# Performance work log

Hardware: AMD Instinct MI355X
Metric: run time of the kernel (lower is better)

Reference implementation:

```python
import jax, jax.numpy as jnp
import numpy as np

D_IN, H1, H2, H3 = 1024, 512, 256, 128  # embedding MLP dims
D_CBP = 2048                             # compact bilinear pooling output dim
H_C = 1024                               # comparator hidden dim
CLASSES = 10
B = 16384
SLOPE = 0.2  # LeakyReLU negative slope


def _lrelu(x):
    return jnp.where(x >= 0, x, SLOPE * x)


def _embed(x, W1, b1, W2, b2, W3, b3):
    x = _lrelu(x @ W1 + b1)
    x = _lrelu(x @ W2 + b2)
    x = _lrelu(x @ W3 + b3)
    return x  # [B, 128]


def setup_inputs() -> dict:
    key = jax.random.key(0)
    ks = jax.random.split(key, 16)

    def lin(k, fan_in, fan_out):
        bound = 1.0 / np.sqrt(fan_in)
        kw, kb = jax.random.split(k)
        W = jax.random.uniform(kw, (fan_in, fan_out), jnp.float32, -bound, bound)
        b = jax.random.uniform(kb, (fan_out,), jnp.float32, -bound, bound)
        return W, b

    W1, b1 = lin(ks[0], D_IN, H1)
    W2, b2 = lin(ks[1], H1, H2)
    W3, b3 = lin(ks[2], H2, H3)
    Wc1, bc1 = lin(ks[3], D_CBP, H_C)
    Wc2, bc2 = lin(ks[4], H_C, CLASSES)

    X = jax.random.normal(ks[5], (B, D_IN), jnp.float32)
    Centers = jax.random.normal(ks[6], (B, D_IN), jnp.float32)

    # count-sketch hashes (int constants) and +-1 signs (float buffers)
    h1 = jax.random.randint(ks[7], (H3,), 0, D_CBP, jnp.int32)
    h2 = jax.random.randint(ks[8], (H3,), 0, D_CBP, jnp.int32)
    s1 = jnp.sign(jax.random.normal(ks[9], (H3,), jnp.float32)) + (jax.random.normal(ks[9], (H3,)) == 0)
    s2 = jnp.sign(jax.random.normal(ks[10], (H3,), jnp.float32)) + (jax.random.normal(ks[10], (H3,)) == 0)

    return {"X": X, "Centers": Centers,
            "W1": W1, "b1": b1, "W2": W2, "b2": b2, "W3": W3, "b3": b3,
            "h1": h1, "s1": s1, "h2": h2, "s2": s2,
            "Wc1": Wc1, "bc1": bc1, "Wc2": Wc2, "bc2": bc2}


def _cbp(x, y, h1, s1, h2, s2):
    # count-sketch via tiny dense sketch matrices [128, 2048]
    M1 = jnp.zeros((H3, D_CBP), x.dtype).at[jnp.arange(H3), h1].set(s1)
    M2 = jnp.zeros((H3, D_CBP), y.dtype).at[jnp.arange(H3), h2].set(s2)
    sk1 = x @ M1  # [B, 2048]
    sk2 = y @ M2
    # circular convolution via real FFT
    return jnp.fft.irfft(jnp.fft.rfft(sk1, axis=-1) * jnp.fft.rfft(sk2, axis=-1), n=D_CBP, axis=-1)


def reference(X, Centers, W1, b1, W2, b2, W3, b3, h1, s1, h2, s2, Wc1, bc1, Wc2, bc2):
    ex = _embed(X, W1, b1, W2, b2, W3, b3)        # [B, 128]
    ec = _embed(Centers, W1, b1, W2, b2, W3, b3)  # [B, 128]
    cbp = _cbp(ex, ec, h1, s1, h2, s2)            # [B, 2048]
    z = _lrelu(cbp @ Wc1 + bc1)                   # [B, 1024]
    logits = z @ Wc2 + bc2                        # [B, classes]
    return jax.nn.softmax(logits, axis=1)
```

## Files before the change

kernel.cpp:

```cpp
#include <hip/hip_runtime.h>
#include <hip/hip_bf16.h>
#include <math.h>

#define BATCH   16384
#define D_IN    1024
#define H1_DIM  512
#define H2_DIM  256
#define H3_DIM  128
#define D_CBP   2048
#define H_C     1024
#define CLASSES 10
#define SLOPE   0.2f

#define NK_PAD  1088
#define NF      (2 * NK_PAD)
#define NF_USED 2080

typedef short v8s __attribute__((ext_vector_type(8)));
typedef float v4f __attribute__((ext_vector_type(4)));
typedef unsigned short u16;
typedef unsigned int   u32;

__device__ __forceinline__ float b2f(unsigned short u) {
  return __uint_as_float(((unsigned)u) << 16);
}
__device__ __forceinline__ u16 f2b(float f) {
  __hip_bfloat16 h = __float2bfloat16(f);
  return __builtin_bit_cast(unsigned short, h);
}

__device__ __forceinline__ float2 twiddle(int idx) {
  const float ang = 6.2831853071795864769f * (float)idx / 2048.f;
  return make_float2(__cosf(ang), __sinf(ang));
}

__device__ __forceinline__ void g2l16(const void* g, void* l) {
  __builtin_amdgcn_global_load_lds(
      (const __attribute__((address_space(1))) void*)g,
      (__attribute__((address_space(3))) void*)l, 16, 0, 0);
}

__global__ __launch_bounds__(256) void gemm_bf16(
    const u16* __restrict__ A,
    const u16* __restrict__ Bt,
    const float* __restrict__ bias,
    u16* __restrict__ C,
    int M, int N, int K, int lda, int ldb, float slope)
{
  __shared__ __align__(16) short Asb[5][128 * 32];
  __shared__ __align__(16) short Bsb[5][128 * 32];

  const int tid  = threadIdx.x;
  const int wave = tid >> 6, lane = tid & 63;
  const int wm = wave >> 1, wn = wave & 1;
  const int u = lane & 15, quad = lane >> 4;

  const int nwg = gridDim.x * gridDim.y;
  int id = blockIdx.y * gridDim.x + blockIdx.x;
  if ((nwg & 7) == 0) id = (id & 7) * (nwg >> 3) + (id >> 3);
  const int m0 = (id / gridDim.x) * 128, n0 = (id % gridDim.x) * 128;

  const int g_log = ((lane & 3) - ((lane >> 3) & 3)) & 3;
  const int srow  = wave * 32 + (lane >> 2);
  const u16* gA0 = A  + (size_t)(m0 + srow)      * lda + g_log * 8;
  const u16* gA1 = A  + (size_t)(m0 + srow + 16) * lda + g_log * 8;
  const u16* gB0 = Bt + (size_t)(n0 + srow)      * ldb + g_log * 8;
  const u16* gB1 = Bt + (size_t)(n0 + srow + 16) * ldb + g_log * 8;
  const int lo0 = (wave * 32)      * 32;
  const int lo1 = (wave * 32 + 16) * 32;

  const int gran = (quad + (u >> 1)) & 3;
  int offA[4], offB[4];
#pragma unroll
  for (int i = 0; i < 4; ++i) {
    offA[i] = (wm * 64 + i * 16 + u) * 32 + gran * 8;
    offB[i] = (wn * 64 + i * 16 + u) * 32 + gran * 8;
  }

  v4f acc[4][4];
#pragma unroll
  for (int i = 0; i < 4; ++i)
#pragma unroll
    for (int j = 0; j < 4; ++j) acc[i][j] = (v4f){0.f, 0.f, 0.f, 0.f};

  const int nsteps = K >> 5;

  auto stage = [&](int s, int buf) {
    const int k0 = s * 32;
    g2l16(gA0 + k0, &Asb[buf][lo0]);
    g2l16(gA1 + k0, &Asb[buf][lo1]);
    g2l16(gB0 + k0, &Bsb[buf][lo0]);
    g2l16(gB1 + k0, &Bsb[buf][lo1]);
  };

  stage(0, 0);
  if (nsteps > 1) stage(1, 1);
  if (nsteps > 2) stage(2, 2);

  int cb = 0, sb = 3;
  for (int t = 0; t < nsteps; ++t) {
    if (t + 3 < nsteps) stage(t + 3, sb);

    const int rem = nsteps - 1 - t;
    if (rem >= 3)      asm volatile("s_waitcnt vmcnt(12)" ::: "memory");
    else if (rem == 2) asm volatile("s_waitcnt vmcnt(8)"  ::: "memory");
    else if (rem == 1) asm volatile("s_waitcnt vmcnt(4)"  ::: "memory");
    else               asm volatile("s_waitcnt vmcnt(0)"  ::: "memory");
    __builtin_amdgcn_s_barrier();
    asm volatile("" ::: "memory");

    v8s a[4], b[4];
#pragma unroll
    for (int i = 0; i < 4; ++i) a[i] = *(const v8s*)&Asb[cb][offA[i]];
#pragma unroll
    for (int j = 0; j < 4; ++j) b[j] = *(const v8s*)&Bsb[cb][offB[j]];
    __builtin_amdgcn_s_setprio(1);
#pragma unroll
    for (int i = 0; i < 4; ++i)
#pragma unroll
      for (int j = 0; j < 4; ++j)
        acc[i][j] = __builtin_amdgcn_mfma_f32_16x16x32_bf16(a[i], b[j], acc[i][j], 0, 0, 0);
    __builtin_amdgcn_s_setprio(0);

    cb = (cb == 4) ? 0 : cb + 1;
    sb = (sb == 4) ? 0 : sb + 1;
  }

  float bcol[4];
#pragma unroll
  for (int j = 0; j < 4; ++j) bcol[j] = bias[n0 + wn * 64 + j * 16 + u];
#pragma unroll
  for (int i = 0; i < 4; ++i)
#pragma unroll
    for (int r = 0; r < 4; ++r) {
      const size_t ro = (size_t)(m0 + wm * 64 + i * 16 + quad * 4 + r) * N
                        + n0 + wn * 64 + u;
#pragma unroll
      for (int j = 0; j < 4; ++j) {
        float v = acc[i][j][r] + bcol[j];
        v = v >= 0.f ? v : slope * v;
        C[ro + j * 16] = f2b(v);
      }
    }
}

__global__ __launch_bounds__(512) void gemm256_bf16(
    const u16* __restrict__ A,
    const u16* __restrict__ Bt,
    const float* __restrict__ bias,
    u16* __restrict__ C,
    int M, int N, int K, int lda, int ldb, float slope)
{
  __shared__ __align__(16) short Asb[4][256 * 32];
  __shared__ __align__(16) short Bsb[4][256 * 32];

  const int tid  = threadIdx.x;
  const int wave = tid >> 6, lane = tid & 63;
  const int wm = wave >> 2, wn = wave & 3;
  const int u = lane & 15, quad = lane >> 4;

  const int nwg = gridDim.x * gridDim.y;
  int id = blockIdx.y * gridDim.x + blockIdx.x;
  if ((nwg & 7) == 0) id = (id & 7) * (nwg >> 3) + (id >> 3);
  const int m0 = (id / gridDim.x) * 256, n0 = (id % gridDim.x) * 256;

  const int g_log = ((lane & 3) - ((lane >> 3) & 3)) & 3;
  const int srow  = wave * 32 + (lane >> 2);
  const u16* gA0 = A  + (size_t)(m0 + srow)      * lda + g_log * 8;
  const u16* gA1 = A  + (size_t)(m0 + srow + 16) * lda + g_log * 8;
  const u16* gB0 = Bt + (size_t)(n0 + srow)      * ldb + g_log * 8;
  const u16* gB1 = Bt + (size_t)(n0 + srow + 16) * ldb + g_log * 8;
  const int lo0 = (wave * 32)      * 32;
  const int lo1 = (wave * 32 + 16) * 32;

  const int gran = (quad + (u >> 1)) & 3;
  int offA[8], offB[4];
#pragma unroll
  for (int i = 0; i < 8; ++i)
    offA[i] = (wm * 128 + i * 16 + u) * 32 + gran * 8;
#pragma unroll
  for (int j = 0; j < 4; ++j)
    offB[j] = (wn * 64 + j * 16 + u) * 32 + gran * 8;

  v4f acc[8][4];
#pragma unroll
  for (int i = 0; i < 8; ++i)
#pragma unroll
    for (int j = 0; j < 4; ++j) acc[i][j] = (v4f){0.f, 0.f, 0.f, 0.f};

  const int nsteps = K >> 5;

  auto stage = [&](int s, int buf) {
    const int k0 = s * 32;
    g2l16(gA0 + k0, &Asb[buf][lo0]);
    g2l16(gA1 + k0, &Asb[buf][lo1]);
    g2l16(gB0 + k0, &Bsb[buf][lo0]);
    g2l16(gB1 + k0, &Bsb[buf][lo1]);
  };

  stage(0, 0);
  if (nsteps > 1) stage(1, 1);

  for (int t = 0; t < nsteps; ++t) {
    if (t + 2 < nsteps) stage(t + 2, (t + 2) & 3);

    const int rem = nsteps - 1 - t;
    if (rem >= 2)      asm volatile("s_waitcnt vmcnt(8)" ::: "memory");
    else if (rem == 1) asm volatile("s_waitcnt vmcnt(4)" ::: "memory");
    else               asm volatile("s_waitcnt vmcnt(0)" ::: "memory");
    __builtin_amdgcn_s_barrier();
    asm volatile("" ::: "memory");

    const int cb = t & 3;
    v8s a[8], b[4];
#pragma unroll
    for (int i = 0; i < 8; ++i) a[i] = *(const v8s*)&Asb[cb][offA[i]];
#pragma unroll
    for (int j = 0; j < 4; ++j) b[j] = *(const v8s*)&Bsb[cb][offB[j]];
    __builtin_amdgcn_s_setprio(1);
#pragma unroll
    for (int i = 0; i < 8; ++i)
#pragma unroll
      for (int j = 0; j < 4; ++j)
        acc[i][j] = __builtin_amdgcn_mfma_f32_16x16x32_bf16(a[i], b[j], acc[i][j], 0, 0, 0);
    __builtin_amdgcn_s_setprio(0);
  }

  float bcol[4];
#pragma unroll
  for (int j = 0; j < 4; ++j) bcol[j] = bias[n0 + wn * 64 + j * 16 + u];
#pragma unroll
  for (int i = 0; i < 8; ++i)
#pragma unroll
    for (int r = 0; r < 4; ++r) {
      const size_t ro = (size_t)(m0 + wm * 128 + i * 16 + quad * 4 + r) * N
                        + n0 + wn * 64 + u;
#pragma unroll
      for (int j = 0; j < 4; ++j) {
        float v = acc[i][j][r] + bcol[j];
        v = v >= 0.f ? v : slope * v;
        C[ro + j * 16] = f2b(v);
      }
    }
}

__device__ __forceinline__ void f_pass(
    const u16* gA0, const u16* gA1, const u16* gB0, const u16* gB1,
    short (*Asb)[128 * 32], short (*Bsb)[128 * 32],
    int lo0, int lo1, const int* offA, const int* offB,
    v4f (&acc)[4][4])
{
  auto stage = [&](int s, int buf) {
    const int k0 = s * 32;
    g2l16(gA0 + k0, &Asb[buf][lo0]);
    g2l16(gA1 + k0, &Asb[buf][lo1]);
    g2l16(gB0 + k0, &Bsb[buf][lo0]);
    g2l16(gB1 + k0, &Bsb[buf][lo1]);
  };
  stage(0, 0); stage(1, 1); stage(2, 2);
#pragma unroll
  for (int t = 0; t < 4; ++t) {
    if (t == 0) stage(3, 3);
    if (t == 0)      asm volatile("s_waitcnt vmcnt(12)" ::: "memory");
    else if (t == 1) asm volatile("s_waitcnt vmcnt(8)"  ::: "memory");
    else if (t == 2) asm volatile("s_waitcnt vmcnt(4)"  ::: "memory");
    else             asm volatile("s_waitcnt vmcnt(0)"  ::: "memory");
    __builtin_amdgcn_s_barrier();
    asm volatile("" ::: "memory");
    v8s a[4], b[4];
#pragma unroll
    for (int i = 0; i < 4; ++i) a[i] = *(const v8s*)&Asb[t][offA[i]];
#pragma unroll
    for (int j = 0; j < 4; ++j) b[j] = *(const v8s*)&Bsb[t][offB[j]];
    __builtin_amdgcn_s_setprio(1);
#pragma unroll
    for (int i = 0; i < 4; ++i)
#pragma unroll
      for (int j = 0; j < 4; ++j)
        acc[i][j] = __builtin_amdgcn_mfma_f32_16x16x32_bf16(a[i], b[j], acc[i][j], 0, 0, 0);
    __builtin_amdgcn_s_setprio(0);
  }
}

__global__ __launch_bounds__(256) void gemm_f1f2(
    const u16* __restrict__ E3,
    const u16* __restrict__ C1t,
    const u16* __restrict__ C2t,
    u16* __restrict__ F1)
{
  __shared__ __align__(16) short Asb[5][128 * 32];
  __shared__ __align__(16) short Bsb[5][128 * 32];

  const int tid  = threadIdx.x;
  const int wave = tid >> 6, lane = tid & 63;
  const int wm = wave >> 1, wn = wave & 1;
  const int u = lane & 15, quad = lane >> 4;
  const int N = NF, K = H3_DIM;

  const int nwg = gridDim.x * gridDim.y;
  int id = blockIdx.y * gridDim.x + blockIdx.x;
  if ((nwg & 7) == 0) id = (id & 7) * (nwg >> 3) + (id >> 3);
  const int m0 = (id / gridDim.x) * 128, n0 = (id % gridDim.x) * 128;

  const int g_log = ((lane & 3) - ((lane >> 3) & 3)) & 3;
  const int srow  = wave * 32 + (lane >> 2);
  const size_t aoffX = (size_t)(m0 + srow) * K + g_log * 8;
  const size_t boff  = (size_t)(n0 + srow) * K + g_log * 8;
  const int lo0 = (wave * 32)      * 32;
  const int lo1 = (wave * 32 + 16) * 32;

  const int gran = (quad + (u >> 1)) & 3;
  int offA[4], offB[4];
#pragma unroll
  for (int i = 0; i < 4; ++i) {
    offA[i] = (wm * 64 + i * 16 + u) * 32 + gran * 8;
    offB[i] = (wn * 64 + i * 16 + u) * 32 + gran * 8;
  }

  v4f acc1[4][4], acc2[4][4];
#pragma unroll
  for (int i = 0; i < 4; ++i)
#pragma unroll
    for (int j = 0; j < 4; ++j) {
      acc1[i][j] = (v4f){0.f, 0.f, 0.f, 0.f};
      acc2[i][j] = (v4f){0.f, 0.f, 0.f, 0.f};
    }

  f_pass(E3 + aoffX, E3 + aoffX + (size_t)16 * K,
         C1t + boff, C1t + boff + (size_t)16 * K,
         Asb, Bsb, lo0, lo1, offA, offB, acc1);
  const size_t aoffC = aoffX + (size_t)BATCH * K;
  f_pass(E3 + aoffC, E3 + aoffC + (size_t)16 * K,
         C2t + boff, C2t + boff + (size_t)16 * K,
         Asb, Bsb, lo0, lo1, offA, offB, acc2);

  const bool im = (u & 1);
#pragma unroll
  for (int i = 0; i < 4; ++i)
#pragma unroll
    for (int r = 0; r < 4; ++r) {
      const size_t ro = (size_t)(m0 + wm * 64 + i * 16 + quad * 4 + r) * N
                        + n0 + wn * 64 + u;
#pragma unroll
      for (int j = 0; j < 4; ++j) {
        const float f1v = acc1[i][j][r];
        const float f1p = __shfl_xor(f1v, 1, 64);
        const float f2v = acc2[i][j][r];
        const float f2p = __shfl_xor(f2v, 1, 64);
        const float outv = im ? (f1p * f2v + f1v * f2p)
                              : (f1v * f2v - f1p * f2p);
        F1[ro + j * 16] = f2b(outv);
      }
    }
}

#define CAST_NB   (BATCH * D_IN / 4 / 256)
#define NB_CAST   (2 * CAST_NB)
#define NB_TW1    ((D_IN / 32) * (H1_DIM / 32))
#define NB_TW2    ((H1_DIM / 32) * (H2_DIM / 32))
#define NB_TW3    ((H2_DIM / 32) * (H3_DIM / 32))
#define NB_TWC1   ((D_CBP / 32) * (H_C / 32))
#define NB_TRANS  (NB_TW1 + NB_TW2 + NB_TW3 + NB_TWC1)
#define NB_GENC   (NF * H3_DIM / 256)
#define NB_GENT   (NF)
#define NB_ZB     9
#define NB_PREP   (NB_CAST + NB_TRANS + NB_GENC + NB_GENT + NB_ZB)

__global__ __launch_bounds__(256) void prep_all(
    const float* __restrict__ X, const float* __restrict__ Centers,
    u16* __restrict__ Xb,
    const float* __restrict__ W1, u16* __restrict__ W1t,
    const float* __restrict__ W2, u16* __restrict__ W2t,
    const float* __restrict__ W3, u16* __restrict__ W3t,
    const float* __restrict__ Wc1, u16* __restrict__ Wc1t,
    const int* __restrict__ h1, const float* __restrict__ s1,
    const int* __restrict__ h2, const float* __restrict__ s2,
    u16* __restrict__ C1t, u16* __restrict__ C2t,
    u16* __restrict__ Tt, float* __restrict__ zbias)
{
  __shared__ float tile[32][33];
  int bx = blockIdx.x;
  const int t = threadIdx.x;

  if (bx < NB_CAST) {
    const float* s = (bx < CAST_NB) ? X : Centers;
    const int i = ((bx < CAST_NB) ? bx : bx - CAST_NB) * 256 + t;
    u16* d = Xb + ((bx < CAST_NB) ? 0 : (size_t)BATCH * D_IN);
    const float4 v = ((const float4*)s)[i];
    __align__(8) u16 o[4] = {f2b(v.x), f2b(v.y), f2b(v.z), f2b(v.w)};
    *(uint2*)(d + (size_t)i * 4) = *(uint2*)o;
    return;
  }
  bx -= NB_CAST;

  if (bx < NB_TRANS) {
    const float* W; u16* Wt; int K, N;
    if (bx < NB_TW1)        { W = W1;  Wt = W1t;  K = D_IN;   N = H1_DIM; }
    else if (bx < NB_TW1 + NB_TW2) {
      bx -= NB_TW1;           W = W2;  Wt = W2t;  K = H1_DIM; N = H2_DIM; }
    else if (bx < NB_TW1 + NB_TW2 + NB_TW3) {
      bx -= NB_TW1 + NB_TW2;  W = W3;  Wt = W3t;  K = H2_DIM; N = H3_DIM; }
    else {
      bx -= NB_TW1 + NB_TW2 + NB_TW3;
                              W = Wc1; Wt = Wc1t; K = D_CBP;  N = H_C;    }
    const int nt = N / 32;
    const int k0 = (bx / nt) * 32, n0 = (bx % nt) * 32;
    const int tx = t & 31, ty = t >> 5;
#pragma unroll
    for (int s = 0; s < 4; ++s) {
      const int k = ty * 4 + s;
      tile[k][tx] = W[(size_t)(k0 + k) * N + n0 + tx];
    }
    __syncthreads();
#pragma unroll
    for (int s = 0; s < 4; ++s) {
      const int n = ty * 4 + s;
      Wt[(size_t)(n0 + n) * K + k0 + tx] = f2b(tile[tx][n]);
    }
    return;
  }
  bx -= NB_TRANS;

  if (bx < NB_GENC) {
    const int id = bx * 256 + t;
    const int m = id >> 7, i = id & 127;
    const int k = m >> 1;
    float v1 = 0.f, v2 = 0.f;
    if (m < 2 * (D_CBP / 2 + 1)) {
      const float2 c1 = twiddle((k * h1[i]) & (D_CBP - 1));
      const float2 c2 = twiddle((k * h2[i]) & (D_CBP - 1));
      v1 = (m & 1) ? -s1[i] * c1.y : s1[i] * c1.x;
      v2 = (m & 1) ? -s2[i] * c2.y : s2[i] * c2.x;
    }
    C1t[id] = f2b(v1);
    C2t[id] = f2b(v2);
    return;
  }
  bx -= NB_GENC;

  if (bx < NB_GENT) {
    const int id = bx * 256 + t;
    const int m = id >> 8, q0 = (id & 255) * 8;
    const int k = m >> 1;
    const float sc = ((k == 0) || (k == D_CBP / 2)) ? (1.f / D_CBP)
                                                    : (2.f / D_CBP);
    __align__(16) u16 o[8];
#pragma unroll
    for (int j = 0; j < 8; ++j) {
      float v = 0.f;
      if (m < 2 * (D_CBP / 2 + 1)) {
        const float2 cs = twiddle((k * (q0 + j)) & (D_CBP - 1));
        v = (m & 1) ? -sc * cs.y : sc * cs.x;
      }
      o[j] = f2b(v);
    }
    *(v8s*)&Tt[(size_t)m * D_CBP + q0] = *(v8s*)o;
    return;
  }
  bx -= NB_GENT;

  {
    const int i = bx * 256 + t;
    if (i < NF) zbias[i] = 0.f;
  }
}

__global__ __launch_bounds__(256) void head_softmax(
    const u16* __restrict__ Z, const float* __restrict__ Wc2,
    const float* __restrict__ bc2, float* __restrict__ out)
{
  const int row  = blockIdx.x * 4 + (threadIdx.x >> 6);
  const int lane = threadIdx.x & 63;

  float acc[CLASSES];
#pragma unroll
  for (int c = 0; c < CLASSES; ++c) acc[c] = 0.f;

  const u16* z = Z + (size_t)row * H_C;
  for (int k = lane; k < H_C; k += 64) {
    const float zv = b2f(z[k]);
    const float* w = Wc2 + (size_t)k * CLASSES;
#pragma unroll
    for (int c = 0; c < CLASSES; ++c) acc[c] += zv * w[c];
  }
#pragma unroll
  for (int c = 0; c < CLASSES; ++c) {
#pragma unroll
    for (int off = 32; off > 0; off >>= 1)
      acc[c] += __shfl_down(acc[c], off);
  }
  if (lane == 0) {
    float l[CLASSES], mx = -1e30f;
#pragma unroll
    for (int c = 0; c < CLASSES; ++c) { l[c] = acc[c] + bc2[c]; mx = fmaxf(mx, l[c]); }
    float s = 0.f;
#pragma unroll
    for (int c = 0; c < CLASSES; ++c) { l[c] = __expf(l[c] - mx); s += l[c]; }
    const float inv = 1.f / s;
#pragma unroll
    for (int c = 0; c < CLASSES; ++c) out[(size_t)row * CLASSES + c] = l[c] * inv;
  }
}

extern "C" void kernel_launch(void* const* d_in, const int* in_sizes, int n_in,
                              void* d_out, int out_size, void* d_ws, size_t ws_size,
                              hipStream_t stream) {
  const float* X       = (const float*)d_in[0];
  const float* Centers = (const float*)d_in[1];
  const float* W1      = (const float*)d_in[2];
  const float* b1      = (const float*)d_in[3];
  const float* W2      = (const float*)d_in[4];
  const float* b2      = (const float*)d_in[5];
  const float* W3      = (const float*)d_in[6];
  const float* b3      = (const float*)d_in[7];
  const int*   h1      = (const int*)d_in[8];
  const float* s1      = (const float*)d_in[9];
  const int*   h2      = (const int*)d_in[10];
  const float* s2      = (const float*)d_in[11];
  const float* Wc1     = (const float*)d_in[12];
  const float* bc1     = (const float*)d_in[13];
  const float* Wc2     = (const float*)d_in[14];
  const float* bc2     = (const float*)d_in[15];
  float* out = (float*)d_out;

  char* ws = (char*)d_ws;
  const size_t MB = 1u << 20;
  const size_t KB = 1u << 10;
  u16*    Xb    = (u16*)(ws);
  u16*    FWt   = (u16*)(ws + 8 * MB + 512 * KB);
  u16*    F1    = (u16*)(ws + 13 * MB);
  u16*    E1b   = (u16*)(ws + 64 * MB);
  u16*    Zb    = (u16*)(ws + 81 * MB);
  u16*    E2b   = (u16*)(ws + 96 * MB);
  u16*    Tt    = (u16*)(ws + 96 * MB);
  u16*    E3b   = (u16*)(ws + 113 * MB);
  u16*    W1t   = (u16*)(ws + 121 * MB);
  u16*    W2t   = (u16*)(ws + 122 * MB);
  u16*    W3t   = (u16*)(ws + 122 * MB + 256 * KB);
  u16*    Wc1t  = (u16*)(ws + 122 * MB + 512 * KB);
  u16*    C1t   = (u16*)(ws + 126 * MB + 512 * KB);
  u16*    C2t   = (u16*)(ws + 127 * MB + 64 * KB);
  float*  zbias = (float*)(ws + 127 * MB + 672 * KB);

  const dim3 blk(256), blk512(512);

  prep_all<<<dim3(NB_PREP), blk, 0, stream>>>(
      X, Centers, Xb, W1, W1t, W2, W2t, W3, W3t, Wc1, Wc1t,
      h1, s1, h2, s2, C1t, C2t, Tt, zbias);

  gemm256_bf16<<<dim3(H1_DIM / 256, 2 * BATCH / 256), blk512, 0, stream>>>(
      Xb, W1t, b1, E1b, 2 * BATCH, H1_DIM, D_IN, D_IN, D_IN, SLOPE);

  gemm_bf16<<<dim3(NF / 128, H_C / 128), blk, 0, stream>>>(
      Wc1t, Tt, zbias, FWt, H_C, NF, D_CBP, D_CBP, D_CBP, 1.0f);

  gemm_bf16<<<dim3(H2_DIM / 128, 2 * BATCH / 128), blk, 0, stream>>>(
      E1b, W2t, b2, E2b, 2 * BATCH, H2_DIM, H1_DIM, H1_DIM, H1_DIM, SLOPE);
  gemm_bf16<<<dim3(H3_DIM / 128, 2 * BATCH / 128), blk, 0, stream>>>(
      E2b, W3t, b3, E3b, 2 * BATCH, H3_DIM, H2_DIM, H2_DIM, H2_DIM, SLOPE);

  gemm_f1f2<<<dim3(NF / 128, BATCH / 128), blk, 0, stream>>>(
      E3b, C1t, C2t, F1);

  gemm256_bf16<<<dim3(H_C / 256, BATCH / 256), blk512, 0, stream>>>(
      F1, FWt, bc1, Zb, BATCH, H_C, NF_USED, NF, NF, SLOPE);

  head_softmax<<<dim3(BATCH / 4), blk, 0, stream>>>(Zb, Wc2, bc2, out);
}
```

Measured before the change: 433.4 us.

## Deepen GEMM prefetch to three stages and double-buffer LDS fragments in registers

Restructures the GEMM main loop so global-to-LDS loads run three k-steps ahead instead of two. The LDS fragment reads for the next step are issued before the current step's MFMAs, so LDS latency overlaps matrix math. This costs an extra set of fragment registers (a_n/b_n), which adds register pressure and may lower occupancy. With four LDS buffers, the write for step t+3 lands in the buffer read at step t-1; ordering depends on the single barrier per iteration.

```diff
diff --git a/kernel.cpp b/kernel.cpp
--- a/kernel.cpp
+++ b/kernel.cpp
@@ -190,40 +190,59 @@
 
   const int nsteps = K >> 5;
 
-  auto stage = [&](int s, int buf) {
-    const int k0 = s * 32;
+  auto stage = [&](int s) {
+    const int k0 = s * 32, buf = s & 3;
     g2l16(gA0 + k0, &Asb[buf][lo0]);
     g2l16(gA1 + k0, &Asb[buf][lo1]);
     g2l16(gB0 + k0, &Bsb[buf][lo0]);
     g2l16(gB1 + k0, &Bsb[buf][lo1]);
   };
 
-  stage(0, 0);
-  if (nsteps > 1) stage(1, 1);
+  stage(0);
+  if (nsteps > 1) stage(1);
+  if (nsteps > 2) stage(2);
+  if (nsteps > 2)      asm volatile("s_waitcnt vmcnt(8)" ::: "memory");
+  else if (nsteps > 1) asm volatile("s_waitcnt vmcnt(4)" ::: "memory");
+  else                 asm volatile("s_waitcnt vmcnt(0)" ::: "memory");
+  __builtin_amdgcn_s_barrier();
+  asm volatile("" ::: "memory");
+
+  v8s a_c[8], b_c[4], a_n[8], b_n[4];
+#pragma unroll
+  for (int i = 0; i < 8; ++i) a_c[i] = *(const v8s*)&Asb[0][offA[i]];
+#pragma unroll
+  for (int j = 0; j < 4; ++j) b_c[j] = *(const v8s*)&Bsb[0][offB[j]];
 
   for (int t = 0; t < nsteps; ++t) {
-    if (t + 2 < nsteps) stage(t + 2, (t + 2) & 3);
-
     const int rem = nsteps - 1 - t;
-    if (rem >= 2)      asm volatile("s_waitcnt vmcnt(8)" ::: "memory");
-    else if (rem == 1) asm volatile("s_waitcnt vmcnt(4)" ::: "memory");
-    else               asm volatile("s_waitcnt vmcnt(0)" ::: "memory");
-    __builtin_amdgcn_s_barrier();
-    asm volatile("" ::: "memory");
-
-    const int cb = t & 3;
-    v8s a[8], b[4];
-#pragma unroll
-    for (int i = 0; i < 8; ++i) a[i] = *(const v8s*)&Asb[cb][offA[i]];
-#pragma unroll
-    for (int j = 0; j < 4; ++j) b[j] = *(const v8s*)&Bsb[cb][offB[j]];
+    if (rem > 0) {
+      if (rem >= 2) asm volatile("s_waitcnt vmcnt(4)" ::: "memory");
+      else          asm volatile("s_waitcnt vmcnt(0)" ::: "memory");
+      __builtin_amdgcn_s_barrier();
+      asm volatile("" ::: "memory");
+      const int nb = (t + 1) & 3;
+#pragma unroll
+      for (int i = 0; i < 8; ++i) a_n[i] = *(const v8s*)&Asb[nb][offA[i]];
+#pragma unroll
+      for (int j = 0; j < 4; ++j) b_n[j] = *(const v8s*)&Bsb[nb][offB[j]];
+    }
+
     __builtin_amdgcn_s_setprio(1);
 #pragma unroll
     for (int i = 0; i < 8; ++i)
 #pragma unroll
       for (int j = 0; j < 4; ++j)
-        acc[i][j] = __builtin_amdgcn_mfma_f32_16x16x32_bf16(a[i], b[j], acc[i][j], 0, 0, 0);
+        acc[i][j] = __builtin_amdgcn_mfma_f32_16x16x32_bf16(a_c[i], b_c[j], acc[i][j], 0, 0, 0);
     __builtin_amdgcn_s_setprio(0);
+
+    if (t + 3 < nsteps) stage(t + 3);
+
+    if (rem > 0) {
+#pragma unroll
+      for (int i = 0; i < 8; ++i) a_c[i] = a_n[i];
+#pragma unroll
+      for (int j = 0; j < 4; ++j) b_c[j] = b_n[j];
+    }
   }
 
   float bcol[4];
```

Result: no change. 428.3 us (-1.2%).
